# Performance work log

Measured on AMD Instinct MI355X. Metric: run time of the kernel, lower is better.

## Reference

```python
import jax, jax.numpy as jnp
import numpy as np

NUM_HEADS = 12
SEQ_H = 32
SEQ_W = 32
D_HALF = 32
ROPE_BASE = 10000.0
LN_EPS = 1e-5


def build_rope_cache(seq_len, head_dim, base=ROPE_BASE):
    inv_freq = 1.0 / base ** (jnp.arange(0, head_dim, 2, dtype=jnp.float32) / head_dim)
    t = jnp.arange(seq_len, dtype=jnp.float32)
    freqs = jnp.outer(t, inv_freq)  # [seq_len, head_dim//2]
    cos = jnp.repeat(jnp.cos(freqs), 2, axis=-1)  # [seq_len, head_dim]
    sin = jnp.repeat(jnp.sin(freqs), 2, axis=-1)
    return cos, sin


def apply_rope(x, cos, sin):
    # x: [B,H,N,d_sub], cos/sin: [N,d_sub]
    x_even, x_odd = x[..., ::2], x[..., 1::2]
    x_rot = jnp.stack([-x_odd, x_even], axis=-1).reshape(x.shape)
    return x * cos[None, None] + x_rot * sin[None, None]


def setup_inputs() -> dict:
    key = jax.random.key(0)
    ks = jax.random.split(key, 3)
    B, N, D = 8, 1025, 768
    return {
        "x": jax.random.normal(ks[0], (B, N, D), dtype=jnp.float32),
        "ln_g": jnp.ones((D,), dtype=jnp.float32),
        "ln_b": jnp.zeros((D,), dtype=jnp.float32),
        "w_qkv": jax.random.normal(ks[1], (3 * D, D), dtype=jnp.float32) * 0.02,
        "w_proj": jax.random.normal(ks[2], (D, D), dtype=jnp.float32) * 0.02,
        "b_proj": jnp.zeros((D,), dtype=jnp.float32),
    }


def reference(x, ln_g, ln_b, w_qkv, w_proj, b_proj):
    B, N, D = x.shape
    H = NUM_HEADS
    hd = D // H
    d2 = D_HALF
    scale = hd ** -0.5

    # LayerNorm
    mu = jnp.mean(x, axis=-1, keepdims=True)
    var = jnp.mean(jnp.square(x - mu), axis=-1, keepdims=True)
    xn = (x - mu) * jax.lax.rsqrt(var + LN_EPS) * ln_g + ln_b

    # QKV projection (no bias)
    qkv = jnp.einsum("bnd,ed->bne", xn, w_qkv).reshape(B, N, 3, H, hd)
    qkv = jnp.transpose(qkv, (2, 0, 3, 1, 4))  # [3,B,H,N,hd]
    q, k, v = qkv[0], qkv[1], qkv[2]

    # 2D position ids (CLS token -> row 0, col 0)
    patch_lin = jnp.arange(N - 1)
    rows = patch_lin // SEQ_W
    cols = patch_lin % SEQ_W
    zero = jnp.zeros((1,), dtype=patch_lin.dtype)
    row_ids = jnp.concatenate([zero, rows])
    col_ids = jnp.concatenate([zero, cols])

    cos_row, sin_row = build_rope_cache(SEQ_H, d2)
    cos_col, sin_col = build_rope_cache(SEQ_W, d2)
    cos_r, sin_r = cos_row[row_ids], sin_row[row_ids]  # [N,d2]
    cos_c, sin_c = cos_col[col_ids], sin_col[col_ids]

    q = jnp.concatenate(
        [apply_rope(q[..., :d2], cos_r, sin_r), apply_rope(q[..., d2:], cos_c, sin_c)], axis=-1)
    k = jnp.concatenate(
        [apply_rope(k[..., :d2], cos_r, sin_r), apply_rope(k[..., d2:], cos_c, sin_c)], axis=-1)

    attn = jnp.einsum("bhqd,bhkd->bhqk", q, k) * scale
    attn = jax.nn.softmax(attn, axis=-1)
    out = jnp.einsum("bhqk,bhkd->bhqd", attn, v)  # [B,H,N,hd]
    out = jnp.transpose(out, (0, 2, 1, 3)).reshape(B, N, D)
    return jnp.einsum("bnd,ed->bne", out, w_proj) + b_proj
```

## Files before the change

### kernel.cpp

```cpp
#include <hip/hip_runtime.h>
#include <hip/hip_bf16.h>

typedef unsigned short u16;

#define B_      8
#define N_      1025
#define D_      768
#define H_      12
#define HD_     64
#define M_REAL  (B_ * N_)
#define M_PAD   8320
#define QKVC    (3 * D_)

typedef __attribute__((ext_vector_type(8))) short bf16x8;
typedef __attribute__((ext_vector_type(4))) float f32x4;

static __device__ __forceinline__ float bf2f(u16 u) {
    union { unsigned int i; float f; } v; v.i = ((unsigned int)u) << 16; return v.f;
}
static __device__ __forceinline__ u16 f2bf(float f) {
    union { float f; unsigned int i; } v; v.f = f;
    unsigned int x = v.i;
    return (u16)((x + 0x7fffu + ((x >> 16) & 1u)) >> 16);
}

__global__ __launch_bounds__(256)
void f2b_kernel(const float* __restrict__ in, u16* __restrict__ out, int n)
{
    int i = (blockIdx.x * 256 + threadIdx.x) * 4;
    if (i + 3 < n) {
        float4 v = *(const float4*)(in + i);
        out[i]     = f2bf(v.x);
        out[i + 1] = f2bf(v.y);
        out[i + 2] = f2bf(v.z);
        out[i + 3] = f2bf(v.w);
    } else {
        for (int j = 0; j < 4 && i + j < n; j++) out[i + j] = f2bf(in[i + j]);
    }
}

__global__ __launch_bounds__(256)
void ln_kernel(const float* __restrict__ x, const float* __restrict__ g,
               const float* __restrict__ bvec, u16* __restrict__ xn)
{
    const int row = blockIdx.x;
    const int tid = threadIdx.x;
    const float* xr = x + (size_t)row * D_;
    float v[3];
    float s = 0.f, ss = 0.f;
#pragma unroll
    for (int j = 0; j < 3; j++) {
        float val = xr[tid + j * 256];
        v[j] = val; s += val; ss += val * val;
    }
    __shared__ float r1[256], r2[256];
    r1[tid] = s; r2[tid] = ss; __syncthreads();
    for (int off = 128; off > 0; off >>= 1) {
        if (tid < off) { r1[tid] += r1[tid + off]; r2[tid] += r2[tid + off]; }
        __syncthreads();
    }
    const float mean = r1[0] * (1.0f / D_);
    const float var  = r2[0] * (1.0f / D_) - mean * mean;
    const float rs   = rsqrtf(var + 1e-5f);
    u16* outr = xn + (size_t)row * D_;
#pragma unroll
    for (int j = 0; j < 3; j++) {
        int c = tid + j * 256;
        outr[c] = f2bf((v[j] - mean) * rs * g[c] + bvec[c]);
    }
}

template <typename OutT, bool ROPE>
__global__ __launch_bounds__(256)
void gemm_bt(const u16* __restrict__ A, const u16* __restrict__ B,
             OutT* __restrict__ C, const float* __restrict__ bias,
             int M_real, int Ncols, int K,
             int BM, int BN, int gh, int gw, int PC)
{
    const int l   = blockIdx.x;
    const int xcd = l & 7;
    const int i0  = l >> 3;
    const int pr  = xcd / PC, pc = xcd % PC;
    const int bm  = pr * gh + (i0 % gh);
    const int bn  = pc * gw + (i0 / gh);
    if (bm >= BM || bn >= BN) return;

    __shared__ __align__(16) u16 As[128 * 40];
    __shared__ __align__(16) u16 Bs[128 * 40];
    const int tid  = threadIdx.x;
    const int wave = tid >> 6, lane = tid & 63;
    const int wm   = (wave >> 1) * 64, wn = (wave & 1) * 64;
    const int lrow = lane & 15, lq = lane >> 4;

    f32x4 acc[4][4];
#pragma unroll
    for (int i = 0; i < 4; i++)
#pragma unroll
        for (int j = 0; j < 4; j++)
            acc[i][j] = (f32x4){0.f, 0.f, 0.f, 0.f};

    const int kTiles = K / 32;
    for (int kt = 0; kt < kTiles; kt++) {
        const int k0 = kt * 32;
#pragma unroll
        for (int i = 0; i < 2; i++) {
            int s   = tid + i * 256;
            int row = s >> 2, cg = (s & 3) * 8;
            int grow = bm * 128 + row;
            uint4 av = make_uint4(0u, 0u, 0u, 0u);
            if (grow < M_real) av = *(const uint4*)(A + (size_t)grow * K + k0 + cg);
            *(uint4*)&As[row * 40 + cg] = av;
            int gcol = bn * 128 + row;
            uint4 bv = *(const uint4*)(B + (size_t)gcol * K + k0 + cg);
            *(uint4*)&Bs[row * 40 + cg] = bv;
        }
        __syncthreads();
        bf16x8 af[4], bfr[4];
#pragma unroll
        for (int i = 0; i < 4; i++) {
            af[i]  = *(const bf16x8*)&As[(wm + i * 16 + lrow) * 40 + lq * 8];
            bfr[i] = *(const bf16x8*)&Bs[(wn + i * 16 + lrow) * 40 + lq * 8];
        }
#pragma unroll
        for (int i = 0; i < 4; i++)
#pragma unroll
            for (int j = 0; j < 4; j++)
                acc[i][j] = __builtin_amdgcn_mfma_f32_16x16x32_bf16(af[i], bfr[j], acc[i][j], 0, 0, 0);
        __syncthreads();
    }

#pragma unroll
    for (int j = 0; j < 4; j++) {
        int gcol = bn * 128 + wn + j * 16 + lrow;
        float bv = bias ? bias[gcol] : 0.f;
        int qk = gcol / D_;
        int dh = gcol & 63;
        int half = dh >> 5, ii = (dh & 31) >> 1;
        float sgn = (dh & 1) ? 1.f : -1.f;
        float invf = exp2f(-(float)ii * 0.8304820237218406f);
#pragma unroll
        for (int i = 0; i < 4; i++) {
            int growbase = bm * 128 + wm + i * 16 + lq * 4;
#pragma unroll
            for (int r = 0; r < 4; r++) {
                int grow = growbase + r;
                float val = acc[i][j][r] + bv;
                if constexpr (ROPE) {
                    if (qk < 2) {
                        float partner = __shfl_xor(val, 1);
                        int n = grow % N_;
                        int pl = n - 1;
                        int pos = (n == 0) ? 0 : (half ? (pl & 31) : (pl >> 5));
                        float ang = (float)pos * invf;
                        val = val * __cosf(ang) + sgn * partner * __sinf(ang);
                    }
                }
                if (grow < M_real) {
                    if constexpr (sizeof(OutT) == 2)
                        C[(size_t)grow * Ncols + gcol] = (OutT)f2bf(val);
                    else
                        C[(size_t)grow * Ncols + gcol] = (OutT)val;
                }
            }
        }
    }
}

__global__ __launch_bounds__(256)
void attn_mfma(const u16* __restrict__ qkv, u16* __restrict__ out)
{
    __shared__ __align__(16) u16 Kt[64][72];
    __shared__ __align__(16) u16 Vt[64][72];
    __shared__ __align__(16) u16 Ps[4][32][72];

    const int l   = blockIdx.x;
    const int xcd = l & 7;
    const int j0  = l >> 3;
    const int bh  = xcd * 12 + j0 / 9;
    const int b  = bh / H_, h = bh % H_;
    const int q0 = (j0 % 9) * 128;
    const int tid  = threadIdx.x;
    const int wave = tid >> 6, lane = tid & 63;
    const int lm = lane & 15, lq = lane >> 4;
    const int qw = q0 + wave * 32;

    bf16x8 qf[2][2];
#pragma unroll
    for (int sq = 0; sq < 2; sq++) {
        int qrow = qw + sq * 16 + lm; if (qrow > N_ - 1) qrow = N_ - 1;
        const u16* qptr = qkv + (size_t)(b * N_ + qrow) * QKVC + h * HD_;
        bf16x8 t0 = *(const bf16x8*)(qptr + lq * 8);
        bf16x8 t1 = *(const bf16x8*)(qptr + 32 + lq * 8);
#pragma unroll
        for (int j = 0; j < 8; j++) {
            t0[j] = (short)f2bf(bf2f((u16)t0[j]) * 0.125f);
            t1[j] = (short)f2bf(bf2f((u16)t1[j]) * 0.125f);
        }
        qf[sq][0] = t0; qf[sq][1] = t1;
    }

    float l_r[2][4];
    f32x4 o_acc[2][4];
#pragma unroll
    for (int sq = 0; sq < 2; sq++)
#pragma unroll
        for (int t = 0; t < 4; t++) {
            l_r[sq][t] = 0.f;
            o_acc[sq][t] = (f32x4){0.f, 0.f, 0.f, 0.f};
        }

    bf16x8 kreg[2], vreg[2];
    {
        int krow = lane; if (krow > N_ - 1) krow = N_ - 1;
        const u16* kvp = qkv + (size_t)(b * N_ + krow) * QKVC + h * HD_;
#pragma unroll
        for (int p = 0; p < 2; p++) {
            int dg = wave + p * 4;
            kreg[p] = *(const bf16x8*)(kvp + D_ + dg * 8);
            vreg[p] = *(const bf16x8*)(kvp + 2 * D_ + dg * 8);
        }
    }

    const int kTiles = (N_ + 63) / 64;
    for (int kt = 0; kt < kTiles; kt++) {
        const int kbase = kt * 64;
        __syncthreads();
#pragma unroll
        for (int p = 0; p < 2; p++) {
            int dg = wave + p * 4;
            *(bf16x8*)&Kt[lane][dg * 8] = kreg[p];
#pragma unroll
            for (int j = 0; j < 8; j++) Vt[dg * 8 + j][lane] = (u16)vreg[p][j];
        }
        __syncthreads();

        if (kt + 1 < kTiles) {
            int krow = kbase + 64 + lane; if (krow > N_ - 1) krow = N_ - 1;
            const u16* kvp = qkv + (size_t)(b * N_ + krow) * QKVC + h * HD_;
#pragma unroll
            for (int p = 0; p < 2; p++) {
                int dg = wave + p * 4;
                kreg[p] = *(const bf16x8*)(kvp + D_ + dg * 8);
                vreg[p] = *(const bf16x8*)(kvp + 2 * D_ + dg * 8);
            }
        }

        f32x4 sc[2][4];
#pragma unroll
        for (int st = 0; st < 4; st++) {
            bf16x8 kf0 = *(const bf16x8*)&Kt[st * 16 + lm][lq * 8];
            bf16x8 kf1 = *(const bf16x8*)&Kt[st * 16 + lm][32 + lq * 8];
#pragma unroll
            for (int sq = 0; sq < 2; sq++) {
                f32x4 s4 = (f32x4){0.f, 0.f, 0.f, 0.f};
                s4 = __builtin_amdgcn_mfma_f32_16x16x32_bf16(qf[sq][0], kf0, s4, 0, 0, 0);
                s4 = __builtin_amdgcn_mfma_f32_16x16x32_bf16(qf[sq][1], kf1, s4, 0, 0, 0);
                sc[sq][st] = s4;
            }
        }

#pragma unroll
        for (int st = 0; st < 4; st++) {
            bool ok = (kbase + st * 16 + lm) < N_;
#pragma unroll
            for (int sq = 0; sq < 2; sq++)
#pragma unroll
                for (int r = 0; r < 4; r++) {
                    float p = ok ? __expf(sc[sq][st][r]) : 0.f;
                    l_r[sq][r] += p;
                    Ps[wave][sq * 16 + lq * 4 + r][st * 16 + lm] = f2bf(p);
                }
        }
        asm volatile("s_waitcnt lgkmcnt(0)" ::: "memory");

        bf16x8 pa[2][2];
#pragma unroll
        for (int sq = 0; sq < 2; sq++) {
            pa[sq][0] = *(const bf16x8*)&Ps[wave][sq * 16 + lm][lq * 8];
            pa[sq][1] = *(const bf16x8*)&Ps[wave][sq * 16 + lm][32 + lq * 8];
        }
#pragma unroll
        for (int nt = 0; nt < 4; nt++) {
            bf16x8 vb0 = *(const bf16x8*)&Vt[nt * 16 + lm][lq * 8];
            bf16x8 vb1 = *(const bf16x8*)&Vt[nt * 16 + lm][32 + lq * 8];
#pragma unroll
            for (int sq = 0; sq < 2; sq++) {
                o_acc[sq][nt] = __builtin_amdgcn_mfma_f32_16x16x32_bf16(pa[sq][0], vb0, o_acc[sq][nt], 0, 0, 0);
                o_acc[sq][nt] = __builtin_amdgcn_mfma_f32_16x16x32_bf16(pa[sq][1], vb1, o_acc[sq][nt], 0, 0, 0);
            }
        }
    }

#pragma unroll
    for (int sq = 0; sq < 2; sq++)
#pragma unroll
        for (int r = 0; r < 4; r++) {
            float l2 = l_r[sq][r];
            l2 += __shfl_xor(l2, 1);
            l2 += __shfl_xor(l2, 2);
            l2 += __shfl_xor(l2, 4);
            l2 += __shfl_xor(l2, 8);
            int q = qw + sq * 16 + lq * 4 + r;
            if (q < N_) {
                float inv = 1.0f / l2;
                u16* orow = out + (size_t)(b * N_ + q) * D_ + h * HD_ + lm;
#pragma unroll
                for (int nt = 0; nt < 4; nt++)
                    orow[nt * 16] = f2bf(o_acc[sq][nt][r] * inv);
            }
        }
}

extern "C" void kernel_launch(void* const* d_in, const int* in_sizes, int n_in,
                              void* d_out, int out_size, void* d_ws, size_t ws_size,
                              hipStream_t stream)
{
    const float* x      = (const float*)d_in[0];
    const float* ln_g   = (const float*)d_in[1];
    const float* ln_b   = (const float*)d_in[2];
    const float* w_qkv  = (const float*)d_in[3];
    const float* w_proj = (const float*)d_in[4];
    const float* b_proj = (const float*)d_in[5];

    u16* wqkv_b  = (u16*)d_ws;
    u16* wproj_b = wqkv_b + (size_t)QKVC * D_;
    u16* xn      = wproj_b + (size_t)D_ * D_;
    u16* qkv     = xn + (size_t)M_PAD * D_;
    u16* attno   = xn;

    f2b_kernel<<<(QKVC * D_) / 1024, 256, 0, stream>>>(w_qkv, wqkv_b, QKVC * D_);
    f2b_kernel<<<(D_ * D_) / 1024, 256, 0, stream>>>(w_proj, wproj_b, D_ * D_);

    ln_kernel<<<M_REAL, 256, 0, stream>>>(x, ln_g, ln_b, xn);

    gemm_bt<u16, true><<<1224, 256, 0, stream>>>(
        xn, wqkv_b, qkv, nullptr, M_REAL, QKVC, D_,
        65, 18, 17, 9, 2);

    attn_mfma<<<864, 256, 0, stream>>>(qkv, attno);

    gemm_bt<float, false><<<432, 256, 0, stream>>>(
        attno, wproj_b, (float*)d_out, b_proj, M_REAL, D_, D_,
        65, 6, 9, 6, 1);
}
```

Baseline: 257.1 us.

## Use direct global-to-LDS loads and stage GEMM epilogue through shared memory

Tile loads in the bf16 GEMM now use global_load_lds, which writes 16-byte chunks straight into unpadded LDS and skips the register round trip. Out-of-range A rows are clamped to the last valid row instead of zero-filled. The epilogue writes bias/RoPE results into a padded LDS tile, which is then written to global memory with coalesced 16-byte stores instead of scattered scalar stores. The trade-offs are unpadded LDS tiles, which may cause bank conflicts on the fragment reads, and extra synchronisation in the staged epilogue.

```diff
diff --git a/kernel.cpp b/kernel.cpp
--- a/kernel.cpp
+++ b/kernel.cpp
@@ -22,6 +22,12 @@
     union { float f; unsigned int i; } v; v.f = f;
     unsigned int x = v.i;
     return (u16)((x + 0x7fffu + ((x >> 16) & 1u)) >> 16);
+}
+
+static __device__ __forceinline__ void g2l16(const u16* g, u16* l) {
+    __builtin_amdgcn_global_load_lds(
+        (const __attribute__((address_space(1))) unsigned int*)g,
+        (__attribute__((address_space(3))) unsigned int*)l, 16, 0, 0);
 }
 
 __global__ __launch_bounds__(256)
@@ -85,12 +91,17 @@
     const int bn  = pc * gw + (i0 / gh);
     if (bm >= BM || bn >= BN) return;
 
-    __shared__ __align__(16) u16 As[128 * 40];
-    __shared__ __align__(16) u16 Bs[128 * 40];
+    __shared__ __align__(16) unsigned char smem[17408];
+    u16*   As   = (u16*)smem;
+    u16*   Bs   = (u16*)(smem + 8192);
+    u16*   ep16 = (u16*)smem;
+    float* ep32 = (float*)smem;
+
     const int tid  = threadIdx.x;
     const int wave = tid >> 6, lane = tid & 63;
     const int wm   = (wave >> 1) * 64, wn = (wave & 1) * 64;
     const int lrow = lane & 15, lq = lane >> 4;
+    const int lrow4 = lane >> 2, lchunk = lane & 3;
 
     f32x4 acc[4][4];
 #pragma unroll
@@ -103,23 +114,21 @@
     for (int kt = 0; kt < kTiles; kt++) {
         const int k0 = kt * 32;
 #pragma unroll
-        for (int i = 0; i < 2; i++) {
-            int s   = tid + i * 256;
-            int row = s >> 2, cg = (s & 3) * 8;
-            int grow = bm * 128 + row;
-            uint4 av = make_uint4(0u, 0u, 0u, 0u);
-            if (grow < M_real) av = *(const uint4*)(A + (size_t)grow * K + k0 + cg);
-            *(uint4*)&As[row * 40 + cg] = av;
-            int gcol = bn * 128 + row;
-            uint4 bv = *(const uint4*)(B + (size_t)gcol * K + k0 + cg);
-            *(uint4*)&Bs[row * 40 + cg] = bv;
-        }
-        __syncthreads();
+        for (int p = 0; p < 2; p++) {
+            int g = wave + p * 4;
+            int arow = bm * 128 + g * 16 + lrow4;
+            if (arow >= M_real) arow = M_real - 1;
+            g2l16(A + (size_t)arow * K + k0 + lchunk * 8, As + g * 512);
+            int brow = bn * 128 + g * 16 + lrow4;
+            g2l16(B + (size_t)brow * K + k0 + lchunk * 8, Bs + g * 512);
+        }
+        __syncthreads();
+
         bf16x8 af[4], bfr[4];
 #pragma unroll
         for (int i = 0; i < 4; i++) {
-            af[i]  = *(const bf16x8*)&As[(wm + i * 16 + lrow) * 40 + lq * 8];
-            bfr[i] = *(const bf16x8*)&Bs[(wn + i * 16 + lrow) * 40 + lq * 8];
+            af[i]  = *(const bf16x8*)&As[(wm + i * 16 + lrow) * 32 + lq * 8];
+            bfr[i] = *(const bf16x8*)&Bs[(wn + i * 16 + lrow) * 32 + lq * 8];
         }
 #pragma unroll
         for (int i = 0; i < 4; i++)
@@ -129,38 +138,80 @@
         __syncthreads();
     }
 
-#pragma unroll
-    for (int j = 0; j < 4; j++) {
-        int gcol = bn * 128 + wn + j * 16 + lrow;
-        float bv = bias ? bias[gcol] : 0.f;
-        int qk = gcol / D_;
-        int dh = gcol & 63;
-        int half = dh >> 5, ii = (dh & 31) >> 1;
-        float sgn = (dh & 1) ? 1.f : -1.f;
-        float invf = exp2f(-(float)ii * 0.8304820237218406f);
-#pragma unroll
-        for (int i = 0; i < 4; i++) {
-            int growbase = bm * 128 + wm + i * 16 + lq * 4;
-#pragma unroll
-            for (int r = 0; r < 4; r++) {
-                int grow = growbase + r;
-                float val = acc[i][j][r] + bv;
-                if constexpr (ROPE) {
-                    if (qk < 2) {
-                        float partner = __shfl_xor(val, 1);
-                        int n = grow % N_;
-                        int pl = n - 1;
-                        int pos = (n == 0) ? 0 : (half ? (pl & 31) : (pl >> 5));
-                        float ang = (float)pos * invf;
-                        val = val * __cosf(ang) + sgn * partner * __sinf(ang);
+    if constexpr (sizeof(OutT) == 2) {
+#pragma unroll
+        for (int s = 0; s < 2; s++) {
+            if (s) __syncthreads();
+            if (wm == s * 64) {
+#pragma unroll
+                for (int j = 0; j < 4; j++) {
+                    int gcol = bn * 128 + wn + j * 16 + lrow;
+                    float bv = bias ? bias[gcol] : 0.f;
+                    int qk = gcol / D_;
+                    int dh = gcol & 63;
+                    int half = dh >> 5, ii = (dh & 31) >> 1;
+                    float sgn = (dh & 1) ? 1.f : -1.f;
+                    float invf = exp2f(-(float)ii * 0.8304820237218406f);
+#pragma unroll
+                    for (int i = 0; i < 4; i++)
+#pragma unroll
+                        for (int r = 0; r < 4; r++) {
+                            int grow = bm * 128 + wm + i * 16 + lq * 4 + r;
+                            float val = acc[i][j][r] + bv;
+                            if constexpr (ROPE) {
+                                if (qk < 2) {
+                                    float partner = __shfl_xor(val, 1);
+                                    int n = grow % N_;
+                                    int pl = n - 1;
+                                    int pos = (n == 0) ? 0 : (half ? (pl & 31) : (pl >> 5));
+                                    float ang = (float)pos * invf;
+                                    val = val * __cosf(ang) + sgn * partner * __sinf(ang);
+                                }
+                            }
+                            ep16[(i * 16 + lq * 4 + r) * 136 + wn + j * 16 + lrow] = f2bf(val);
+                        }
+                }
+            }
+            __syncthreads();
+#pragma unroll
+            for (int c = 0; c < 4; c++) {
+                int idx = tid + c * 256;
+                int row = idx >> 4, l16 = idx & 15;
+                int grow = bm * 128 + s * 64 + row;
+                if (grow < M_real)
+                    *(uint4*)((u16*)C + (size_t)grow * Ncols + bn * 128 + l16 * 8) =
+                        *(const uint4*)&ep16[row * 136 + l16 * 8];
+            }
+        }
+    } else {
+#pragma unroll
+        for (int s = 0; s < 4; s++) {
+            if (s) __syncthreads();
+            if (wm == (s >> 1) * 64) {
+                int ibase = (s & 1) * 2;
+#pragma unroll
+                for (int j = 0; j < 4; j++) {
+                    int gcol = bn * 128 + wn + j * 16 + lrow;
+                    float bv = bias ? bias[gcol] : 0.f;
+#pragma unroll
+                    for (int io = 0; io < 2; io++) {
+                        int i = ibase + io;
+#pragma unroll
+                        for (int r = 0; r < 4; r++)
+                            ep32[(io * 16 + lq * 4 + r) * 132 + wn + j * 16 + lrow] =
+                                acc[i][j][r] + bv;
                     }
                 }
-                if (grow < M_real) {
-                    if constexpr (sizeof(OutT) == 2)
-                        C[(size_t)grow * Ncols + gcol] = (OutT)f2bf(val);
-                    else
-                        C[(size_t)grow * Ncols + gcol] = (OutT)val;
-                }
+            }
+            __syncthreads();
+#pragma unroll
+            for (int c = 0; c < 4; c++) {
+                int idx = tid + c * 256;
+                int row = idx >> 5, l32 = idx & 31;
+                int grow = bm * 128 + s * 32 + row;
+                if (grow < M_real)
+                    *(uint4*)((float*)C + (size_t)grow * Ncols + bn * 128 + l32 * 4) =
+                        *(const uint4*)&ep32[row * 132 + l32 * 4];
             }
         }
     }
```

Measured after the change: 257.2 us. Within noise of the previous version (+0.0%).
